# Optimization experiments

Hardware: AMD Instinct MI355X
Metric: run time of the kernel (lower is better)

## Reference

```python
import jax, jax.numpy as jnp
import numpy as np

N_NODES = 100000
N_EDGES = 1200000
D = 64

def _mlp(x, w1, b1, w2, b2):
    # Linear -> tanh -> Linear (hidden activation tanh, no output activation)
    h = jnp.tanh(x @ w1 + b1)
    return h @ w2 + b2

def setup_inputs() -> dict:
    key = jax.random.key(0)
    ks = jax.random.split(key, 12)
    s = 1.0 / np.sqrt(D)
    inp = {
        "idx_i": jax.random.randint(ks[0], (N_EDGES,), 0, N_NODES, dtype=jnp.int32),
        "idx_j": jax.random.randint(ks[1], (N_EDGES,), 0, N_NODES, dtype=jnp.int32),
        "p1": jax.random.normal(ks[2], (N_NODES, D), dtype=jnp.float32),
        "basis": jax.random.normal(ks[3], (N_EDGES, D), dtype=jnp.float32),
    }
    names = ["pp_w1", "pp_w2", "pi_w1", "pi_w2", "ii_w1", "ii_w2"]
    for i, nm in enumerate(names):
        inp[nm] = jax.random.normal(ks[4 + i], (D, D), dtype=jnp.float32) * s
    for nm in ["pp_b1", "pp_b2", "pi_b1", "pi_b2", "ii_b1", "ii_b2"]:
        inp[nm] = jnp.zeros((D,), dtype=jnp.float32)
    return inp

def reference(idx_i, idx_j, p1, basis,
              pp_w1, pp_b1, pp_w2, pp_b2,
              pi_w1, pi_b1, pi_w2, pi_b2,
              ii_w1, ii_b1, ii_w2, ii_b2):
    # pp: per-node MLP
    pp1 = _mlp(p1, pp_w1, pp_b1, pp_w2, pp_b2)            # [N, D]
    # pi: gather both endpoints, fuse with basis, per-edge MLP
    inter = pp1[idx_i] + basis + pp1[idx_j]               # [E, D]
    pi1 = _mlp(inter, pi_w1, pi_b1, pi_w2, pi_b2)         # [E, D]
    # ii: per-edge MLP
    ii1 = _mlp(pi1, ii_w1, ii_b1, ii_w2, ii_b2)           # [E, D]
    # ip: scatter-add edge messages back to nodes
    ip1 = jax.ops.segment_sum(ii1, idx_i, num_segments=N_NODES)  # [N, D]
    return ip1
```

## Files before the change

### kernel.cpp

```cpp
#include <hip/hip_runtime.h>
#include <hip/hip_bf16.h>

#define DD 64

using f32x4 = __attribute__((ext_vector_type(4))) float;
using bfrag = __attribute__((ext_vector_type(8))) short;
using u32x4 = __attribute__((ext_vector_type(4))) unsigned int;

__device__ __forceinline__ short f2bf(float f) {
    __hip_bfloat16 h = __float2bfloat16(f);
    return *reinterpret_cast<short*>(&h);
}
__device__ __forceinline__ unsigned cvtpk(float a, float b) {
    unsigned r;
    asm("v_cvt_pk_bf16_f32 %0, %1, %2" : "=v"(r) : "v"(a), "v"(b));
    return r;
}
__device__ __forceinline__ float tanh_fast(float x) {
    float e = __expf(-2.f * x);
    return __fdividef(2.f, 1.f + e) - 1.f;
}
template <int CTRL>
__device__ __forceinline__ int dpp_i(int x) {
    return __builtin_amdgcn_update_dpp(0, x, CTRL, 0xF, 0xF, true);
}
template <int CTRL>
__device__ __forceinline__ float dpp_f(float x) {
    return __int_as_float(__builtin_amdgcn_update_dpp(0, __float_as_int(x), CTRL, 0xF, 0xF, true));
}

__global__ __launch_bounds__(256) void prep_weights(
    const float* __restrict__ w0, const float* __restrict__ w1,
    const float* __restrict__ w2, const float* __restrict__ w3,
    const float* __restrict__ w4, const float* __restrict__ w5,
    unsigned short* __restrict__ wfrag,
    float4* __restrict__ out4, int out_elems4,
    int* __restrict__ counts, int n_nodes)
{
    int gid = blockIdx.x * 256 + threadIdx.x;
    int gsz = gridDim.x * 256;
    for (int i = gid; i < out_elems4; i += gsz)
        out4[i] = make_float4(0.f, 0.f, 0.f, 0.f);
    for (int i = gid; i < n_nodes; i += gsz) counts[i] = 0;
    const float* W[6] = {w0, w1, w2, w3, w4, w5};
    for (int t = gid; t < 6 * 4096; t += gsz) {
        int l = t >> 12, r = t & 4095;
        int j = r & 7, lane = (r >> 3) & 63, ks = (r >> 9) & 1, dt = r >> 10;
        int k = ks * 32 + (lane >> 4) * 8 + j;
        int d = dt * 16 + (lane & 15);
        wfrag[t] = (unsigned short)f2bf(W[l][k * DD + d]);
    }
}

__device__ __forceinline__ void mfma_layer(const unsigned short* __restrict__ s_w, int layer,
                                           int lane, const float* __restrict__ s_bias, int g,
                                           bfrag B0, bfrag B1, f32x4 acc[4])
{
#pragma unroll
    for (int dt = 0; dt < 4; ++dt) {
        f32x4 a = *(const f32x4*)&s_bias[dt * 16 + g * 4];
        bfrag A0 = *(const bfrag*)&s_w[(layer * 8 + dt * 2 + 0) * 512 + lane * 8];
        bfrag A1 = *(const bfrag*)&s_w[(layer * 8 + dt * 2 + 1) * 512 + lane * 8];
        a = __builtin_amdgcn_mfma_f32_16x16x32_bf16(A0, B0, a, 0, 0, 0);
        a = __builtin_amdgcn_mfma_f32_16x16x32_bf16(A1, B1, a, 0, 0, 0);
        acc[dt] = a;
    }
}

template <bool ACT>
__device__ __forceinline__ void h_roundtrip(char* H, int swz, int m, int g,
                                            f32x4 acc[4], bfrag B[2])
{
#pragma unroll
    for (int dt = 0; dt < 4; ++dt) {
        float t0, t1, t2, t3;
        if (ACT) {
            t0 = tanh_fast(acc[dt][0]); t1 = tanh_fast(acc[dt][1]);
            t2 = tanh_fast(acc[dt][2]); t3 = tanh_fast(acc[dt][3]);
        } else {
            t0 = acc[dt][0]; t1 = acc[dt][1]; t2 = acc[dt][2]; t3 = acc[dt][3];
        }
        uint2 w;
        w.x = cvtpk(t0, t1);
        w.y = cvtpk(t2, t3);
        *(uint2*)(H + ((m * 128 + dt * 32 + g * 8) ^ swz)) = w;
    }
#pragma unroll
    for (int ks = 0; ks < 2; ++ks)
        B[ks] = *(const bfrag*)(H + ((m * 128 + ks * 64 + g * 16) ^ swz));
}

__global__ __launch_bounds__(256) void node_mfma_kernel(
    const float* __restrict__ p1,
    const unsigned short* __restrict__ wfrag,
    const float* __restrict__ b1, const float* __restrict__ b2,
    unsigned short* __restrict__ pp1, int n_rows)
{
    __shared__ __align__(16) unsigned short s_w[2 * 4096];
    __shared__ __align__(16) float s_b[2][DD];
    __shared__ __align__(16) unsigned short s_h[4][1024];

    int tid = threadIdx.x;
    {
        const u32x4* src = (const u32x4*)wfrag;
        u32x4* dst = (u32x4*)s_w;
        for (int i = tid; i < 2 * 4096 / 8; i += 256) dst[i] = src[i];
    }
    if (tid < DD) { s_b[0][tid] = b1[tid]; s_b[1][tid] = b2[tid]; }
    __syncthreads();

    int wave = tid >> 6, lane = tid & 63;
    int g = lane >> 4, m = lane & 15;
    char* H = (char*)s_h[wave];
    int swz = (m & 7) << 4;

    int gw = blockIdx.x * 4 + wave;
    int nw = gridDim.x * 4;
    int ntiles = (n_rows + 15) >> 4;

    for (int t = gw; t < ntiles; t += nw) {
        int row = t * 16 + m;
        int rc = min(row, n_rows - 1);
        bfrag B[2];
#pragma unroll
        for (int ks = 0; ks < 2; ++ks) {
            int f0 = ks * 32 + g * 8;
            f32x4 x0 = *(const f32x4*)(p1 + (size_t)rc * DD + f0);
            f32x4 x1 = *(const f32x4*)(p1 + (size_t)rc * DD + f0 + 4);
            u32x4 r;
            r[0] = cvtpk(x0[0], x0[1]);
            r[1] = cvtpk(x0[2], x0[3]);
            r[2] = cvtpk(x1[0], x1[1]);
            r[3] = cvtpk(x1[2], x1[3]);
            B[ks] = *reinterpret_cast<bfrag*>(&r);
        }
        f32x4 acc[4];
        mfma_layer(s_w, 0, lane, s_b[0], g, B[0], B[1], acc);
        h_roundtrip<true>(H, swz, m, g, acc, B);
        mfma_layer(s_w, 1, lane, s_b[1], g, B[0], B[1], acc);
        if (row < n_rows) {
#pragma unroll
            for (int dt = 0; dt < 4; ++dt) {
                unsigned int* dst = (unsigned int*)((char*)pp1 + (size_t)row * 128 + dt * 32 + g * 8);
                dst[0] = cvtpk(acc[dt][0], acc[dt][1]);
                dst[1] = cvtpk(acc[dt][2], acc[dt][3]);
            }
        }
    }
}

__global__ void hist_kernel(const int* __restrict__ idx_i, int* __restrict__ counts, int n) {
    int base = (blockIdx.x * 256 + threadIdx.x) * 4;
    if (base + 3 < n) {
        int4 v = *(const int4*)(idx_i + base);
        atomicAdd(&counts[v.x], 1); atomicAdd(&counts[v.y], 1);
        atomicAdd(&counts[v.z], 1); atomicAdd(&counts[v.w], 1);
    } else {
        for (int e = base; e < n; ++e) atomicAdd(&counts[idx_i[e]], 1);
    }
}

__global__ void chunk_reduce(const int* __restrict__ counts, int* __restrict__ csum, int n) {
    __shared__ int red[256];
    int b = blockIdx.x, t = threadIdx.x;
    int base = b * 1024 + t * 4, s = 0;
#pragma unroll
    for (int j = 0; j < 4; ++j) { int i = base + j; s += (i < n) ? counts[i] : 0; }
    red[t] = s; __syncthreads();
    for (int off = 128; off; off >>= 1) { if (t < off) red[t] += red[t + off]; __syncthreads(); }
    if (!t) csum[b] = red[0];
}

__global__ void chunk_scan(const int* __restrict__ counts, const int* __restrict__ csum,
                           int* __restrict__ cursor, int n, int nch) {
    __shared__ int sbase[256];
    __shared__ int sums[256];
    int b = blockIdx.x, t = threadIdx.x;
    sbase[t] = (t < b && t < nch) ? csum[t] : 0;
    __syncthreads();
    for (int d = 128; d; d >>= 1) { if (t < d) sbase[t] += sbase[t + d]; __syncthreads(); }
    int cbase = sbase[0];

    int base = b * 1024 + t * 4;
    int v[4], s = 0;
#pragma unroll
    for (int j = 0; j < 4; ++j) { v[j] = (base + j < n) ? counts[base + j] : 0; s += v[j]; }
    sums[t] = s; __syncthreads();
    for (int d = 1; d < 256; d <<= 1) {
        int x = sums[t];
        if (t >= d) x += sums[t - d];
        __syncthreads();
        sums[t] = x;
        __syncthreads();
    }
    int excl = sums[t] - s + cbase;
#pragma unroll
    for (int j = 0; j < 4; ++j) {
        if (base + j < n) cursor[base + j] = excl;
        excl += v[j];
    }
}

__global__ void bin_kernel(const int* __restrict__ idx_i, const int* __restrict__ idx_j,
                           int* __restrict__ cursor, int4* __restrict__ sorted, int n) {
    int base = (blockIdx.x * 256 + threadIdx.x) * 4;
    if (base + 3 < n) {
        int4 vi = *(const int4*)(idx_i + base);
        int4 vj = *(const int4*)(idx_j + base);
        int p;
        p = atomicAdd(&cursor[vi.x], 1); sorted[p] = make_int4(vi.x, vj.x, base + 0, 0);
        p = atomicAdd(&cursor[vi.y], 1); sorted[p] = make_int4(vi.y, vj.y, base + 1, 0);
        p = atomicAdd(&cursor[vi.z], 1); sorted[p] = make_int4(vi.z, vj.z, base + 2, 0);
        p = atomicAdd(&cursor[vi.w], 1); sorted[p] = make_int4(vi.w, vj.w, base + 3, 0);
    } else {
        for (int e = base; e < n; ++e) {
            int ni = idx_i[e];
            int p = atomicAdd(&cursor[ni], 1);
            sorted[p] = make_int4(ni, idx_j[e], e, 0);
        }
    }
}

struct Gath {
    u32x4 piA, piB, pjA, pjB;
    f32x4 b0, b1, b2, b3;
};

__device__ __forceinline__ int4 load_rec(const int4* __restrict__ sorted, int t, int m, int n_edges) {
    int gm = t * 16 + m;
    return sorted[min(gm, n_edges - 1)];
}

__device__ __forceinline__ Gath issue_gather(const int4& rec,
                                             const unsigned short* __restrict__ pp1,
                                             const float* __restrict__ basis, int g)
{
    Gath G;
    const unsigned* pi_p = (const unsigned*)(pp1 + (size_t)rec.x * DD);
    const unsigned* pj_p = (const unsigned*)(pp1 + (size_t)rec.y * DD);
    const float* bs = basis + (size_t)rec.z * DD;
    G.piA = *(const u32x4*)(pi_p + g * 4);
    G.piB = *(const u32x4*)(pi_p + 16 + g * 4);
    G.pjA = *(const u32x4*)(pj_p + g * 4);
    G.pjB = *(const u32x4*)(pj_p + 16 + g * 4);
    G.b0 = *(const f32x4*)(bs + g * 8);
    G.b1 = *(const f32x4*)(bs + g * 8 + 4);
    G.b2 = *(const f32x4*)(bs + 32 + g * 8);
    G.b3 = *(const f32x4*)(bs + 32 + g * 8 + 4);
    return G;
}

__device__ __forceinline__ void build_B(const Gath& G, bfrag B[2])
{
    float bf[16];
    *(f32x4*)&bf[0] = G.b0; *(f32x4*)&bf[4] = G.b1;
    *(f32x4*)&bf[8] = G.b2; *(f32x4*)&bf[12] = G.b3;
    u32x4 pi[2] = {G.piA, G.piB};
    u32x4 pj[2] = {G.pjA, G.pjB};
#pragma unroll
    for (int ks = 0; ks < 2; ++ks) {
        u32x4 r;
#pragma unroll
        for (int w = 0; w < 4; ++w) {
            unsigned upi = pi[ks][w], upj = pj[ks][w];
            float lo = __uint_as_float(upi << 16) + bf[ks * 8 + 2 * w]
                     + __uint_as_float(upj << 16);
            float hi = __uint_as_float(upi & 0xFFFF0000u) + bf[ks * 8 + 2 * w + 1]
                     + __uint_as_float(upj & 0xFFFF0000u);
            r[w] = cvtpk(lo, hi);
        }
        B[ks] = *reinterpret_cast<bfrag*>(&r);
    }
}

__global__ __launch_bounds__(256) void edge_sorted_kernel(
    const int4* __restrict__ sorted,
    const unsigned short* __restrict__ pp1,
    const float* __restrict__ basis,
    const unsigned short* __restrict__ wfrag,
    const float* __restrict__ pi_b1, const float* __restrict__ pi_b2,
    const float* __restrict__ ii_b1, const float* __restrict__ ii_b2,
    float* __restrict__ out, int n_edges, int ntiles)
{
    __shared__ __align__(16) unsigned short s_w[4 * 4096];
    __shared__ __align__(16) float s_b[4][DD];
    __shared__ __align__(16) unsigned short s_h[4][1024];

    int tid = threadIdx.x;
    {
        const u32x4* src = (const u32x4*)(wfrag + 2 * 4096);
        u32x4* dst = (u32x4*)s_w;
        for (int i = tid; i < 4 * 4096 / 8; i += 256) dst[i] = src[i];
    }
    if (tid < DD) {
        s_b[0][tid] = pi_b1[tid]; s_b[1][tid] = pi_b2[tid];
        s_b[2][tid] = ii_b1[tid]; s_b[3][tid] = ii_b2[tid];
    }
    __syncthreads();

    int wave = tid >> 6, lane = tid & 63;
    int g = lane >> 4, m = lane & 15;
    char* H = (char*)s_h[wave];
    int swz = (m & 7) << 4;

    int nwaves = gridDim.x * 4;
    int w = blockIdx.x * 4 + wave;
    int tpw = (ntiles + nwaves - 1) / nwaves;
    int t0 = w * tpw;
    int t1 = min(t0 + tpw, ntiles);
    if (t0 >= t1) return;

    int id_before = (t0 > 0) ? sorted[t0 * 16 - 1].x : -2;

    int cur = -9;
    float carry[16];
#pragma unroll
    for (int i = 0; i < 16; ++i) carry[i] = 0.f;

    int4 rec_c = load_rec(sorted, t0, m, n_edges);
    int4 rec_n = load_rec(sorted, t0 + 1, m, n_edges);
    Gath gc = issue_gather(rec_c, pp1, basis, g);

    for (int t = t0; t < t1; ++t) {
        int ne = (t + 1) * 16;
        int nf_raw = __shfl(rec_n.x, 0);
        int next_first = (ne < n_edges) ? nf_raw : -3;

        int gm = t * 16 + m;
        int idv = (gm < n_edges) ? rec_c.x : -1;

        bfrag B[2];
        build_B(gc, B);
        int4 rec_n2 = load_rec(sorted, t + 2, m, n_edges);
        if (t + 1 < t1) gc = issue_gather(rec_n, pp1, basis, g);

        f32x4 acc[4];
        mfma_layer(s_w, 0, lane, s_b[0], g, B[0], B[1], acc);
        h_roundtrip<true>(H, swz, m, g, acc, B);
        mfma_layer(s_w, 1, lane, s_b[1], g, B[0], B[1], acc);
        h_roundtrip<false>(H, swz, m, g, acc, B);
        mfma_layer(s_w, 2, lane, s_b[2], g, B[0], B[1], acc);
        h_roundtrip<true>(H, swz, m, g, acc, B);
        mfma_layer(s_w, 3, lane, s_b[3], g, B[0], B[1], acc);

        float v[16];
#pragma unroll
        for (int i = 0; i < 16; ++i) v[i] = acc[i >> 2][i & 3];

        {
            int idS; float cm;
            idS = dpp_i<0x111>(idv); cm = ((m >= 1) && (idS == idv)) ? 1.f : 0.f;
#pragma unroll
            for (int i = 0; i < 16; ++i) { float sh = dpp_f<0x111>(v[i]); v[i] = fmaf(sh, cm, v[i]); }
            idS = dpp_i<0x112>(idv); cm = ((m >= 2) && (idS == idv)) ? 1.f : 0.f;
#pragma unroll
            for (int i = 0; i < 16; ++i) { float sh = dpp_f<0x112>(v[i]); v[i] = fmaf(sh, cm, v[i]); }
            idS = dpp_i<0x114>(idv); cm = ((m >= 4) && (idS == idv)) ? 1.f : 0.f;
#pragma unroll
            for (int i = 0; i < 16; ++i) { float sh = dpp_f<0x114>(v[i]); v[i] = fmaf(sh, cm, v[i]); }
            idS = dpp_i<0x118>(idv); cm = ((m >= 8) && (idS == idv)) ? 1.f : 0.f;
#pragma unroll
            for (int i = 0; i < 16; ++i) { float sh = dpp_f<0x118>(v[i]); v[i] = fmaf(sh, cm, v[i]); }
        }

        int id_next = dpp_i<0x101>(idv);
        bool last = (m == 15);
        bool closes = last ? (idv != next_first) : (idv != id_next);

        if (closes && idv == cur) {
#pragma unroll
            for (int i = 0; i < 16; ++i) v[i] += carry[i];
        }
        if (closes && idv >= 0) {
            size_t ob = (size_t)idv * DD;
            if (idv > id_before) {
#pragma unroll
                for (int dt = 0; dt < 4; ++dt) {
                    f32x4 sv = {v[dt * 4 + 0], v[dt * 4 + 1], v[dt * 4 + 2], v[dt * 4 + 3]};
                    *(f32x4*)&out[ob + (size_t)(dt * 16 + g * 4)] = sv;
                }
            } else {
#pragma unroll
                for (int i = 0; i < 16; ++i)
                    atomicAdd(&out[ob + (size_t)((i >> 2) * 16 + g * 4 + (i & 3))], v[i]);
            }
        }

        int id15 = __shfl(idv, 15);
        bool cont = (id15 == next_first);
        bool cont_carry = (id15 == cur);
        if (cont) {
#pragma unroll
            for (int i = 0; i < 16; ++i) {
                float s15 = __shfl(v[i], lane | 15);
                carry[i] = s15 + (cont_carry ? carry[i] : 0.f);
            }
        }
        cur = cont ? id15 : -9;

        rec_c = rec_n; rec_n = rec_n2;
    }

    if (cur >= 0 && m == 0) {
#pragma unroll
        for (int i = 0; i < 16; ++i)
            atomicAdd(&out[(size_t)cur * DD + (size_t)((i >> 2) * 16 + g * 4 + (i & 3))], carry[i]);
    }
}

extern "C" void kernel_launch(void* const* d_in, const int* in_sizes, int n_in,
                              void* d_out, int out_size, void* d_ws, size_t ws_size,
                              hipStream_t stream) {
    const int*   idx_i = (const int*)d_in[0];
    const int*   idx_j = (const int*)d_in[1];
    const float* p1    = (const float*)d_in[2];
    const float* basis = (const float*)d_in[3];
    const float* pp_w1 = (const float*)d_in[4];
    const float* pp_w2 = (const float*)d_in[5];
    const float* pi_w1 = (const float*)d_in[6];
    const float* pi_w2 = (const float*)d_in[7];
    const float* ii_w1 = (const float*)d_in[8];
    const float* ii_w2 = (const float*)d_in[9];
    const float* pp_b1 = (const float*)d_in[10];
    const float* pp_b2 = (const float*)d_in[11];
    const float* pi_b1 = (const float*)d_in[12];
    const float* pi_b2 = (const float*)d_in[13];
    const float* ii_b1 = (const float*)d_in[14];
    const float* ii_b2 = (const float*)d_in[15];

    int n_edges = in_sizes[0];
    int n_nodes = in_sizes[2] / DD;
    int ntiles  = (n_edges + 15) / 16;

    size_t off = 0;
    auto take = [&](size_t b) { size_t o = off; off += (b + 255) & ~(size_t)255; return o; };
    size_t o_wfrag  = take(6 * 4096 * 2);
    size_t o_pp1    = take((size_t)n_nodes * DD * 2);
    size_t o_counts = take((size_t)n_nodes * 4);
    size_t o_csum   = take(1024 * 4);
    size_t o_cursor = take((size_t)n_nodes * 4);
    size_t o_sorted = take((size_t)ntiles * 16 * 16);
    (void)off;

    char* ws = (char*)d_ws;
    unsigned short* wfrag  = (unsigned short*)(ws + o_wfrag);
    unsigned short* pp1    = (unsigned short*)(ws + o_pp1);
    int*            counts = (int*)(ws + o_counts);
    int*            csum   = (int*)(ws + o_csum);
    int*            cursor = (int*)(ws + o_cursor);
    int4*           sorted = (int4*)(ws + o_sorted);
    float* out = (float*)d_out;

    prep_weights<<<512, 256, 0, stream>>>(pp_w1, pp_w2, pi_w1, pi_w2, ii_w1, ii_w2,
                                          wfrag, (float4*)out, out_size / 4,
                                          counts, n_nodes);

    node_mfma_kernel<<<512, 256, 0, stream>>>(p1, wfrag, pp_b1, pp_b2, pp1, n_nodes);

    int eg4 = (n_edges / 4 + 255) / 256 + 1;
    int nch = (n_nodes + 1023) / 1024;
    hist_kernel<<<eg4, 256, 0, stream>>>(idx_i, counts, n_edges);
    chunk_reduce<<<nch, 256, 0, stream>>>(counts, csum, n_nodes);
    chunk_scan<<<nch, 256, 0, stream>>>(counts, csum, cursor, n_nodes, nch);
    bin_kernel<<<eg4, 256, 0, stream>>>(idx_i, idx_j, cursor, sorted, n_edges);

    edge_sorted_kernel<<<768, 256, 0, stream>>>(sorted, pp1, basis, wfrag,
                                                pi_b1, pi_b2, ii_b1, ii_b2,
                                                out, n_edges, ntiles);
}
```

Measured before the change: 318.2 us.

## Fuse node MLP, histogram and output zeroing; pack sorted edge records into 64 bits

Merges the node MLP, edge-index histogram and output zeroing into one launch that partitions work by block range, so they run concurrently instead of back to back. The two-pass chunk reduce and scan become one kernel in which each block recomputes its prefix base by summing all earlier counts. Sorted edge records shrink from 16-byte int4 to packed 64-bit (node i, node j, edge id) bitfields, halving the record traffic in binning and in the edge kernel. The trade-off is redundant prefix summing per block and a bit-packing scheme that needs 2*bn plus the edge-id bits to fit in 64.

Measured after the change: 335.6 us. +5.5%, slower.

```diff
diff --git a/kernel.cpp b/kernel.cpp
--- a/kernel.cpp
+++ b/kernel.cpp
@@ -6,6 +6,7 @@
 using f32x4 = __attribute__((ext_vector_type(4))) float;
 using bfrag = __attribute__((ext_vector_type(8))) short;
 using u32x4 = __attribute__((ext_vector_type(4))) unsigned int;
+typedef unsigned long long u64;
 
 __device__ __forceinline__ short f2bf(float f) {
     __hip_bfloat16 h = __float2bfloat16(f);
@@ -34,13 +35,10 @@
     const float* __restrict__ w2, const float* __restrict__ w3,
     const float* __restrict__ w4, const float* __restrict__ w5,
     unsigned short* __restrict__ wfrag,
-    float4* __restrict__ out4, int out_elems4,
     int* __restrict__ counts, int n_nodes)
 {
     int gid = blockIdx.x * 256 + threadIdx.x;
     int gsz = gridDim.x * 256;
-    for (int i = gid; i < out_elems4; i += gsz)
-        out4[i] = make_float4(0.f, 0.f, 0.f, 0.f);
     for (int i = gid; i < n_nodes; i += gsz) counts[i] = 0;
     const float* W[6] = {w0, w1, w2, w3, w4, w5};
     for (int t = gid; t < 6 * 4096; t += gsz) {
@@ -90,96 +88,102 @@
         B[ks] = *(const bfrag*)(H + ((m * 128 + ks * 64 + g * 16) ^ swz));
 }
 
-__global__ __launch_bounds__(256) void node_mfma_kernel(
-    const float* __restrict__ p1,
-    const unsigned short* __restrict__ wfrag,
+__global__ __launch_bounds__(256) void node_hist_zero(
+    const float* __restrict__ p1, const unsigned short* __restrict__ wfrag,
     const float* __restrict__ b1, const float* __restrict__ b2,
-    unsigned short* __restrict__ pp1, int n_rows)
+    unsigned short* __restrict__ pp1, int n_rows,
+    const int* __restrict__ idx_i, int* __restrict__ counts, int n_edges,
+    float4* __restrict__ out4, int out_elems4,
+    int nodeBlocks, int histBlocks, int zeroBlocks)
 {
     __shared__ __align__(16) unsigned short s_w[2 * 4096];
     __shared__ __align__(16) float s_b[2][DD];
     __shared__ __align__(16) unsigned short s_h[4][1024];
 
+    int bid = blockIdx.x;
     int tid = threadIdx.x;
-    {
-        const u32x4* src = (const u32x4*)wfrag;
-        u32x4* dst = (u32x4*)s_w;
-        for (int i = tid; i < 2 * 4096 / 8; i += 256) dst[i] = src[i];
-    }
-    if (tid < DD) { s_b[0][tid] = b1[tid]; s_b[1][tid] = b2[tid]; }
-    __syncthreads();
-
-    int wave = tid >> 6, lane = tid & 63;
-    int g = lane >> 4, m = lane & 15;
-    char* H = (char*)s_h[wave];
-    int swz = (m & 7) << 4;
-
-    int gw = blockIdx.x * 4 + wave;
-    int nw = gridDim.x * 4;
-    int ntiles = (n_rows + 15) >> 4;
-
-    for (int t = gw; t < ntiles; t += nw) {
-        int row = t * 16 + m;
-        int rc = min(row, n_rows - 1);
-        bfrag B[2];
-#pragma unroll
-        for (int ks = 0; ks < 2; ++ks) {
-            int f0 = ks * 32 + g * 8;
-            f32x4 x0 = *(const f32x4*)(p1 + (size_t)rc * DD + f0);
-            f32x4 x1 = *(const f32x4*)(p1 + (size_t)rc * DD + f0 + 4);
-            u32x4 r;
-            r[0] = cvtpk(x0[0], x0[1]);
-            r[1] = cvtpk(x0[2], x0[3]);
-            r[2] = cvtpk(x1[0], x1[1]);
-            r[3] = cvtpk(x1[2], x1[3]);
-            B[ks] = *reinterpret_cast<bfrag*>(&r);
-        }
-        f32x4 acc[4];
-        mfma_layer(s_w, 0, lane, s_b[0], g, B[0], B[1], acc);
-        h_roundtrip<true>(H, swz, m, g, acc, B);
-        mfma_layer(s_w, 1, lane, s_b[1], g, B[0], B[1], acc);
-        if (row < n_rows) {
-#pragma unroll
-            for (int dt = 0; dt < 4; ++dt) {
-                unsigned int* dst = (unsigned int*)((char*)pp1 + (size_t)row * 128 + dt * 32 + g * 8);
-                dst[0] = cvtpk(acc[dt][0], acc[dt][1]);
-                dst[1] = cvtpk(acc[dt][2], acc[dt][3]);
+
+    if (bid < nodeBlocks) {
+        {
+            const u32x4* src = (const u32x4*)wfrag;
+            u32x4* dst = (u32x4*)s_w;
+            for (int i = tid; i < 2 * 4096 / 8; i += 256) dst[i] = src[i];
+        }
+        if (tid < DD) { s_b[0][tid] = b1[tid]; s_b[1][tid] = b2[tid]; }
+        __syncthreads();
+
+        int wave = tid >> 6, lane = tid & 63;
+        int g = lane >> 4, m = lane & 15;
+        char* H = (char*)s_h[wave];
+        int swz = (m & 7) << 4;
+
+        int gw = bid * 4 + wave;
+        int nw = nodeBlocks * 4;
+        int ntiles = (n_rows + 15) >> 4;
+
+        for (int t = gw; t < ntiles; t += nw) {
+            int row = t * 16 + m;
+            int rc = min(row, n_rows - 1);
+            bfrag B[2];
+#pragma unroll
+            for (int ks = 0; ks < 2; ++ks) {
+                int f0 = ks * 32 + g * 8;
+                f32x4 x0 = *(const f32x4*)(p1 + (size_t)rc * DD + f0);
+                f32x4 x1 = *(const f32x4*)(p1 + (size_t)rc * DD + f0 + 4);
+                u32x4 r;
+                r[0] = cvtpk(x0[0], x0[1]);
+                r[1] = cvtpk(x0[2], x0[3]);
+                r[2] = cvtpk(x1[0], x1[1]);
+                r[3] = cvtpk(x1[2], x1[3]);
+                B[ks] = *reinterpret_cast<bfrag*>(&r);
             }
-        }
-    }
-}
-
-__global__ void hist_kernel(const int* __restrict__ idx_i, int* __restrict__ counts, int n) {
-    int base = (blockIdx.x * 256 + threadIdx.x) * 4;
-    if (base + 3 < n) {
-        int4 v = *(const int4*)(idx_i + base);
-        atomicAdd(&counts[v.x], 1); atomicAdd(&counts[v.y], 1);
-        atomicAdd(&counts[v.z], 1); atomicAdd(&counts[v.w], 1);
+            f32x4 acc[4];
+            mfma_layer(s_w, 0, lane, s_b[0], g, B[0], B[1], acc);
+            h_roundtrip<true>(H, swz, m, g, acc, B);
+            mfma_layer(s_w, 1, lane, s_b[1], g, B[0], B[1], acc);
+            if (row < n_rows) {
+#pragma unroll
+                for (int dt = 0; dt < 4; ++dt) {
+                    unsigned int* dst = (unsigned int*)((char*)pp1 + (size_t)row * 128 + dt * 32 + g * 8);
+                    dst[0] = cvtpk(acc[dt][0], acc[dt][1]);
+                    dst[1] = cvtpk(acc[dt][2], acc[dt][3]);
+                }
+            }
+        }
+    } else if (bid < nodeBlocks + histBlocks) {
+        int b = bid - nodeBlocks;
+        int base = (b * 256 + tid) * 4;
+        if (base + 3 < n_edges) {
+            int4 v = *(const int4*)(idx_i + base);
+            atomicAdd(&counts[v.x], 1); atomicAdd(&counts[v.y], 1);
+            atomicAdd(&counts[v.z], 1); atomicAdd(&counts[v.w], 1);
+        } else {
+            for (int e = base; e < n_edges; ++e) atomicAdd(&counts[idx_i[e]], 1);
+        }
     } else {
-        for (int e = base; e < n; ++e) atomicAdd(&counts[idx_i[e]], 1);
-    }
-}
-
-__global__ void chunk_reduce(const int* __restrict__ counts, int* __restrict__ csum, int n) {
+        int b = bid - nodeBlocks - histBlocks;
+        int gid = b * 256 + tid;
+        int gsz = zeroBlocks * 256;
+        for (int i = gid; i < out_elems4; i += gsz)
+            out4[i] = make_float4(0.f, 0.f, 0.f, 0.f);
+    }
+}
+
+__global__ void scan_fused(const int* __restrict__ counts, int* __restrict__ cursor, int n) {
     __shared__ int red[256];
-    int b = blockIdx.x, t = threadIdx.x;
-    int base = b * 1024 + t * 4, s = 0;
-#pragma unroll
-    for (int j = 0; j < 4; ++j) { int i = base + j; s += (i < n) ? counts[i] : 0; }
-    red[t] = s; __syncthreads();
-    for (int off = 128; off; off >>= 1) { if (t < off) red[t] += red[t + off]; __syncthreads(); }
-    if (!t) csum[b] = red[0];
-}
-
-__global__ void chunk_scan(const int* __restrict__ counts, const int* __restrict__ csum,
-                           int* __restrict__ cursor, int n, int nch) {
-    __shared__ int sbase[256];
     __shared__ int sums[256];
     int b = blockIdx.x, t = threadIdx.x;
-    sbase[t] = (t < b && t < nch) ? csum[t] : 0;
+
+    int lim4 = (b * 1024) >> 2;
+    int s0 = 0;
+    for (int i = t; i < lim4; i += 256) {
+        int4 v4 = ((const int4*)counts)[i];
+        s0 += v4.x + v4.y + v4.z + v4.w;
+    }
+    red[t] = s0; __syncthreads();
+    for (int off = 128; off; off >>= 1) { if (t < off) red[t] += red[t + off]; __syncthreads(); }
+    int cbase = red[0];
     __syncthreads();
-    for (int d = 128; d; d >>= 1) { if (t < d) sbase[t] += sbase[t + d]; __syncthreads(); }
-    int cbase = sbase[0];
 
     int base = b * 1024 + t * 4;
     int v[4], s = 0;
@@ -202,21 +206,25 @@
 }
 
 __global__ void bin_kernel(const int* __restrict__ idx_i, const int* __restrict__ idx_j,
-                           int* __restrict__ cursor, int4* __restrict__ sorted, int n) {
+                           int* __restrict__ cursor, u64* __restrict__ sorted, int n, int bn) {
     int base = (blockIdx.x * 256 + threadIdx.x) * 4;
     if (base + 3 < n) {
         int4 vi = *(const int4*)(idx_i + base);
         int4 vj = *(const int4*)(idx_j + base);
         int p;
-        p = atomicAdd(&cursor[vi.x], 1); sorted[p] = make_int4(vi.x, vj.x, base + 0, 0);
-        p = atomicAdd(&cursor[vi.y], 1); sorted[p] = make_int4(vi.y, vj.y, base + 1, 0);
-        p = atomicAdd(&cursor[vi.z], 1); sorted[p] = make_int4(vi.z, vj.z, base + 2, 0);
-        p = atomicAdd(&cursor[vi.w], 1); sorted[p] = make_int4(vi.w, vj.w, base + 3, 0);
+        p = atomicAdd(&cursor[vi.x], 1);
+        sorted[p] = (u64)vi.x | ((u64)vj.x << bn) | ((u64)(base + 0) << (2 * bn));
+        p = atomicAdd(&cursor[vi.y], 1);
+        sorted[p] = (u64)vi.y | ((u64)vj.y << bn) | ((u64)(base + 1) << (2 * bn));
+        p = atomicAdd(&cursor[vi.z], 1);
+        sorted[p] = (u64)vi.z | ((u64)vj.z << bn) | ((u64)(base + 2) << (2 * bn));
+        p = atomicAdd(&cursor[vi.w], 1);
+        sorted[p] = (u64)vi.w | ((u64)vj.w << bn) | ((u64)(base + 3) << (2 * bn));
     } else {
         for (int e = base; e < n; ++e) {
             int ni = idx_i[e];
             int p = atomicAdd(&cursor[ni], 1);
-            sorted[p] = make_int4(ni, idx_j[e], e, 0);
+            sorted[p] = (u64)ni | ((u64)idx_j[e] << bn) | ((u64)e << (2 * bn));
         }
     }
 }
@@ -226,19 +234,22 @@
     f32x4 b0, b1, b2, b3;
 };
 
-__device__ __forceinline__ int4 load_rec(const int4* __restrict__ sorted, int t, int m, int n_edges) {
+__device__ __forceinline__ u64 load_rec(const u64* __restrict__ sorted, int t, int m, int n_edges) {
     int gm = t * 16 + m;
     return sorted[min(gm, n_edges - 1)];
 }
 
-__device__ __forceinline__ Gath issue_gather(const int4& rec,
+__device__ __forceinline__ Gath issue_gather(u64 rec, int bn, unsigned nmask,
                                              const unsigned short* __restrict__ pp1,
                                              const float* __restrict__ basis, int g)
 {
+    int ni = (int)((unsigned)rec & nmask);
+    int nj = (int)((unsigned)(rec >> bn) & nmask);
+    int e  = (int)(rec >> (2 * bn));
     Gath G;
-    const unsigned* pi_p = (const unsigned*)(pp1 + (size_t)rec.x * DD);
-    const unsigned* pj_p = (const unsigned*)(pp1 + (size_t)rec.y * DD);
-    const float* bs = basis + (size_t)rec.z * DD;
+    const unsigned* pi_p = (const unsigned*)(pp1 + (size_t)ni * DD);
+    const unsigned* pj_p = (const unsigned*)(pp1 + (size_t)nj * DD);
+    const float* bs = basis + (size_t)e * DD;
     G.piA = *(const u32x4*)(pi_p + g * 4);
     G.piB = *(const u32x4*)(pi_p + 16 + g * 4);
     G.pjA = *(const u32x4*)(pj_p + g * 4);
@@ -274,17 +285,19 @@
 }
 
 __global__ __launch_bounds__(256) void edge_sorted_kernel(
-    const int4* __restrict__ sorted,
+    const u64* __restrict__ sorted,
     const unsigned short* __restrict__ pp1,
     const float* __restrict__ basis,
     const unsigned short* __restrict__ wfrag,
     const float* __restrict__ pi_b1, const float* __restrict__ pi_b2,
     const float* __restrict__ ii_b1, const float* __restrict__ ii_b2,
-    float* __restrict__ out, int n_edges, int ntiles)
+    float* __restrict__ out, int n_edges, int ntiles, int bn)
 {
     __shared__ __align__(16) unsigned short s_w[4 * 4096];
     __shared__ __align__(16) float s_b[4][DD];
     __shared__ __align__(16) unsigned short s_h[4][1024];
+
+    const unsigned nmask = (1u << bn) - 1u;
 
     int tid = threadIdx.x;
     {
@@ -310,29 +323,29 @@
     int t1 = min(t0 + tpw, ntiles);
     if (t0 >= t1) return;
 
-    int id_before = (t0 > 0) ? sorted[t0 * 16 - 1].x : -2;
+    int id_before = (t0 > 0) ? (int)((unsigned)sorted[t0 * 16 - 1] & nmask) : -2;
 
     int cur = -9;
     float carry[16];
 #pragma unroll
     for (int i = 0; i < 16; ++i) carry[i] = 0.f;
 
-    int4 rec_c = load_rec(sorted, t0, m, n_edges);
-    int4 rec_n = load_rec(sorted, t0 + 1, m, n_edges);
-    Gath gc = issue_gather(rec_c, pp1, basis, g);
+    u64 rec_c = load_rec(sorted, t0, m, n_edges);
+    u64 rec_n = load_rec(sorted, t0 + 1, m, n_edges);
+    Gath gc = issue_gather(rec_c, bn, nmask, pp1, basis, g);
 
     for (int t = t0; t < t1; ++t) {
         int ne = (t + 1) * 16;
-        int nf_raw = __shfl(rec_n.x, 0);
-        int next_first = (ne < n_edges) ? nf_raw : -3;
+        int nf_raw = __shfl((int)(unsigned)rec_n, 0);
+        int next_first = (ne < n_edges) ? (int)((unsigned)nf_raw & nmask) : -3;
 
         int gm = t * 16 + m;
-        int idv = (gm < n_edges) ? rec_c.x : -1;
+        int idv = (gm < n_edges) ? (int)((unsigned)rec_c & nmask) : -1;
 
         bfrag B[2];
         build_B(gc, B);
-        int4 rec_n2 = load_rec(sorted, t + 2, m, n_edges);
-        if (t + 1 < t1) gc = issue_gather(rec_n, pp1, basis, g);
+        u64 rec_n2 = load_rec(sorted, t + 2, m, n_edges);
+        if (t + 1 < t1) gc = issue_gather(rec_n, bn, nmask, pp1, basis, g);
 
         f32x4 acc[4];
         mfma_layer(s_w, 0, lane, s_b[0], g, B[0], B[1], acc);
@@ -432,39 +445,42 @@
     int n_nodes = in_sizes[2] / DD;
     int ntiles  = (n_edges + 15) / 16;
 
+    int bn = 0; while ((1 << bn) < n_nodes) ++bn;
+
     size_t off = 0;
     auto take = [&](size_t b) { size_t o = off; off += (b + 255) & ~(size_t)255; return o; };
     size_t o_wfrag  = take(6 * 4096 * 2);
     size_t o_pp1    = take((size_t)n_nodes * DD * 2);
     size_t o_counts = take((size_t)n_nodes * 4);
-    size_t o_csum   = take(1024 * 4);
     size_t o_cursor = take((size_t)n_nodes * 4);
-    size_t o_sorted = take((size_t)ntiles * 16 * 16);
+    size_t o_sorted = take((size_t)ntiles * 16 * 8);
     (void)off;
 
     char* ws = (char*)d_ws;
     unsigned short* wfrag  = (unsigned short*)(ws + o_wfrag);
     unsigned short* pp1    = (unsigned short*)(ws + o_pp1);
     int*            counts = (int*)(ws + o_counts);
-    int*            csum   = (int*)(ws + o_csum);
     int*            cursor = (int*)(ws + o_cursor);
-    int4*           sorted = (int4*)(ws + o_sorted);
+    u64*            sorted = (u64*)(ws + o_sorted);
     float* out = (float*)d_out;
 
-    prep_weights<<<512, 256, 0, stream>>>(pp_w1, pp_w2, pi_w1, pi_w2, ii_w1, ii_w2,
-                                          wfrag, (float4*)out, out_size / 4,
-                                          counts, n_nodes);
-
-    node_mfma_kernel<<<512, 256, 0, stream>>>(p1, wfrag, pp_b1, pp_b2, pp1, n_nodes);
-
-    int eg4 = (n_edges / 4 + 255) / 256 + 1;
+    prep_weights<<<128, 256, 0, stream>>>(pp_w1, pp_w2, pi_w1, pi_w2, ii_w1, ii_w2,
+                                          wfrag, counts, n_nodes);
+
+    int histBlocks = (n_edges / 4 + 255) / 256 + 1;
+    int nodeBlocks = 512, zeroBlocks = 512;
+    node_hist_zero<<<nodeBlocks + histBlocks + zeroBlocks, 256, 0, stream>>>(
+        p1, wfrag, pp_b1, pp_b2, pp1, n_nodes,
+        idx_i, counts, n_edges,
+        (float4*)out, out_size / 4,
+        nodeBlocks, histBlocks, zeroBlocks);
+
     int nch = (n_nodes + 1023) / 1024;
-    hist_kernel<<<eg4, 256, 0, stream>>>(idx_i, counts, n_edges);
-    chunk_reduce<<<nch, 256, 0, stream>>>(counts, csum, n_nodes);
-    chunk_scan<<<nch, 256, 0, stream>>>(counts, csum, cursor, n_nodes, nch);
-    bin_kernel<<<eg4, 256, 0, stream>>>(idx_i, idx_j, cursor, sorted, n_edges);
+    scan_fused<<<nch, 256, 0, stream>>>(counts, cursor, n_nodes);
+
+    bin_kernel<<<histBlocks, 256, 0, stream>>>(idx_i, idx_j, cursor, sorted, n_edges, bn);
 
     edge_sorted_kernel<<<768, 256, 0, stream>>>(sorted, pp1, basis, wfrag,
                                                 pi_b1, pi_b2, ii_b1, ii_b2,
-                                                out, n_edges, ntiles);
-}
+                                                out, n_edges, ntiles, bn);
+}
```
